# Performance work log

Measured on AMD Instinct MI355X. Metric: run time of the kernel, lower is better.

## Reference

```python
import jax, jax.numpy as jnp
import numpy as np

POOL = 7                     # cfg.POOLING_SIZE
PRE = 2 * POOL               # pre_pool_size (max_pool=True path)
LEVEL_HW = (256, 128, 64, 32)  # square H=W of P2..P5 for a 1024x1024 image


def setup_inputs() -> dict:
    key = jax.random.key(0)
    ks = jax.random.split(key, 8)
    C = 256
    feats = {f"p{i + 2}": jax.random.normal(ks[i], (1, C, s, s), dtype=jnp.float32)
             for i, s in enumerate(LEVEL_HW)}
    N = 1000
    IMG = 1024.0
    x1 = jax.random.uniform(ks[4], (N,), minval=0.0, maxval=IMG - 33.0)
    y1 = jax.random.uniform(ks[5], (N,), minval=0.0, maxval=IMG - 33.0)
    w = jax.random.uniform(ks[6], (N,), minval=32.0, maxval=512.0)
    h = jax.random.uniform(ks[7], (N,), minval=32.0, maxval=512.0)
    x2 = jnp.minimum(x1 + w, IMG - 1.0)
    y2 = jnp.minimum(y1 + h, IMG - 1.0)
    rois = jnp.stack([jnp.zeros((N,), jnp.float32), x1, y1, x2, y2], axis=1)
    inp = dict(feats)
    inp["rois"] = rois
    return inp


def _crop_pool_fpn(p2, p3, p4, p5, rois):
    """Faithful vectorized version of Network._crop_pool_layer_fpn (max_pool=True).

    Per-ROI FPN level select, affine-grid + bilinear grid_sample
    (align_corners=True semantics, zeros padding), then 2x2 max pool.
    """
    levels = (p2, p3, p4, p5)
    C = p2.shape[1]
    Hm = p2.shape[2]  # largest (P2) map; all levels padded up to this
    # Pad every level into one [L, Hm, Wm, C] array (NHWC for clean gathers).
    feats = jnp.stack([
        jnp.pad(jnp.transpose(f[0], (1, 2, 0)),
                ((0, Hm - f.shape[2]), (0, Hm - f.shape[3]), (0, 0)))
        for f in levels])

    x1, y1, x2, y2 = rois[:, 1], rois[:, 2], rois[:, 3], rois[:, 4]
    w = jnp.where(x2 - x1 <= 0, 1e-14, x2 - x1)
    h = jnp.where(y2 - y1 <= 0, 1e-14, y2 - y1)
    kf = 4.0 + jnp.log2(jnp.sqrt(w * h) / 224.0)   # k0 + log2(sqrt(wh)/224)
    kf = jnp.clip(kf, 2.0, 5.0)                     # clamp BEFORE round (as in source)
    k = jnp.round(kf)
    scale = 2.0 ** k
    lvl = k.astype(jnp.int32) - 2                   # [N] in [0,4)
    x1s, y1s, x2s, y2s = x1 / scale, y1 / scale, x2 / scale, y2 / scale

    # affine_grid(theta) + align_corners=True grid_sample collapses to direct
    # pixel coords: px = (x1+x2)/2 + t*(x2-x1)/2, t = linspace(-1, 1, PRE).
    t = jnp.linspace(-1.0, 1.0, PRE)
    px = (x1s + x2s)[:, None] * 0.5 + t[None, :] * ((x2s - x1s)[:, None] * 0.5)  # [N,PRE]
    py = (y1s + y2s)[:, None] * 0.5 + t[None, :] * ((y2s - y1s)[:, None] * 0.5)
    PX = jnp.broadcast_to(px[:, None, :], (px.shape[0], PRE, PRE))  # [N,PRE,PRE]
    PY = jnp.broadcast_to(py[:, :, None], (py.shape[0], PRE, PRE))

    HWl = jnp.asarray(LEVEL_HW, jnp.float32)[lvl][:, None, None]  # per-ROI level size (square)
    x0 = jnp.floor(PX)
    y0 = jnp.floor(PY)
    dx = PX - x0
    dy = PY - y0

    def gather(yi, xi):
        inb = ((xi >= 0) & (xi < HWl) & (yi >= 0) & (yi < HWl)).astype(feats.dtype)
        yc = jnp.clip(yi, 0, Hm - 1).astype(jnp.int32)
        xc = jnp.clip(xi, 0, Hm - 1).astype(jnp.int32)
        v = feats[lvl[:, None, None], yc, xc]      # [N,PRE,PRE,C]
        return v * inb[..., None]                   # zeros padding

    out = (gather(y0, x0) * ((1 - dy) * (1 - dx))[..., None]
           + gather(y0, x0 + 1) * ((1 - dy) * dx)[..., None]
           + gather(y0 + 1, x0) * (dy * (1 - dx))[..., None]
           + gather(y0 + 1, x0 + 1) * (dy * dx)[..., None])  # [N,PRE,PRE,C]

    crops = jnp.transpose(out, (0, 3, 1, 2))        # [N,C,PRE,PRE]
    N = crops.shape[0]
    crops = crops.reshape(N, C, POOL, 2, POOL, 2).max(axis=(3, 5))  # 2x2 max pool
    return crops                                     # [N,C,POOL,POOL]


def reference(p2, p3, p4, p5, rois):
    return _crop_pool_fpn(p2, p3, p4, p5, rois)
```

## Files before the change

### kernel.cpp

```cpp
#include <hip/hip_runtime.h>
#include <math.h>

#define C_CH 256
#define PRE 14
#define NPOOL 7
#define PIX (NPOOL * NPOOL)
#define OUT_PER_ROI (C_CH * PIX)
#define HALF_OUT (128 * PIX)
#define SROW 132

#define OFF_P2 0
#define OFF_P3 16777216u
#define OFF_P4 20971520u
#define OFF_P5 22020096u
#define WS_ELEMS 22282240u

#define RB 528

static __device__ __forceinline__ unsigned short f2bf(float f) {
    unsigned int u = __float_as_uint(f);
    unsigned int r = (u + 0x7FFFu + ((u >> 16) & 1u)) >> 16;
    return (unsigned short)r;
}
static __device__ __forceinline__ float bfLO(unsigned int u) { return __uint_as_float(u << 16); }
static __device__ __forceinline__ float bfHI(unsigned int u) { return __uint_as_float(u & 0xFFFF0000u); }

static __device__ __forceinline__ void bilerp8(uint4 a00, uint4 a01, uint4 a10, uint4 a11,
                                               float4 w, float4& lo, float4& hi) {
    lo.x = fmaf(bfLO(a00.x), w.x, fmaf(bfLO(a01.x), w.y, fmaf(bfLO(a10.x), w.z, bfLO(a11.x) * w.w)));
    lo.y = fmaf(bfHI(a00.x), w.x, fmaf(bfHI(a01.x), w.y, fmaf(bfHI(a10.x), w.z, bfHI(a11.x) * w.w)));
    lo.z = fmaf(bfLO(a00.y), w.x, fmaf(bfLO(a01.y), w.y, fmaf(bfLO(a10.y), w.z, bfLO(a11.y) * w.w)));
    lo.w = fmaf(bfHI(a00.y), w.x, fmaf(bfHI(a01.y), w.y, fmaf(bfHI(a10.y), w.z, bfHI(a11.y) * w.w)));
    hi.x = fmaf(bfLO(a00.z), w.x, fmaf(bfLO(a01.z), w.y, fmaf(bfLO(a10.z), w.z, bfLO(a11.z) * w.w)));
    hi.y = fmaf(bfHI(a00.z), w.x, fmaf(bfHI(a01.z), w.y, fmaf(bfHI(a10.z), w.z, bfHI(a11.z) * w.w)));
    hi.z = fmaf(bfLO(a00.w), w.x, fmaf(bfLO(a01.w), w.y, fmaf(bfLO(a10.w), w.z, bfLO(a11.w) * w.w)));
    hi.w = fmaf(bfHI(a00.w), w.x, fmaf(bfHI(a01.w), w.y, fmaf(bfHI(a10.w), w.z, bfHI(a11.w) * w.w)));
}

__global__ __launch_bounds__(256) void transpose_all_k(
    const float* __restrict__ p2, const float* __restrict__ p3,
    const float* __restrict__ p4, const float* __restrict__ p5,
    unsigned short* __restrict__ ws) {
    __shared__ unsigned char lds[128 * RB];

    int b = blockIdx.x;
    const float* __restrict__ src;
    int HW2; unsigned int off;
    if (b < 512)      { src = p2; HW2 = 65536; off = OFF_P2; }
    else if (b < 640) { src = p3; HW2 = 16384; off = OFF_P3; b -= 512; }
    else if (b < 672) { src = p4; HW2 = 4096;  off = OFF_P4; b -= 640; }
    else              { src = p5; HW2 = 1024;  off = OFF_P5; b -= 672; }
    const int hw0 = b << 7;

    const int t   = threadIdx.x;
    const int hwq = t & 31;
    const int cg  = t >> 5;
    const int key = (hwq & 7) << 4;

    #pragma unroll
    for (int s = 0; s < 8; ++s) {
        const int c0 = (cg << 2) + (s << 5);
        const float* g = src + (size_t)c0 * HW2 + hw0 + (hwq << 2);
        const float4 a0 = *(const float4*)(g);
        const float4 a1 = *(const float4*)(g + HW2);
        const float4 a2 = *(const float4*)(g + 2 * (size_t)HW2);
        const float4 a3 = *(const float4*)(g + 3 * (size_t)HW2);
        const int cb = (c0 << 1) ^ key;
        unsigned char* base = &lds[(hwq << 2) * RB + cb];
        ushort4 w;
        w.x = f2bf(a0.x); w.y = f2bf(a1.x); w.z = f2bf(a2.x); w.w = f2bf(a3.x);
        *(ushort4*)(base) = w;
        w.x = f2bf(a0.y); w.y = f2bf(a1.y); w.z = f2bf(a2.y); w.w = f2bf(a3.y);
        *(ushort4*)(base + RB) = w;
        w.x = f2bf(a0.z); w.y = f2bf(a1.z); w.z = f2bf(a2.z); w.w = f2bf(a3.z);
        *(ushort4*)(base + 2 * RB) = w;
        w.x = f2bf(a0.w); w.y = f2bf(a1.w); w.z = f2bf(a2.w); w.w = f2bf(a3.w);
        *(ushort4*)(base + 3 * RB) = w;
    }
    __syncthreads();

    char* __restrict__ dstb = (char*)(ws + off + ((size_t)hw0 << 8));
    const int chunk = t & 31;
    const int hwl   = t >> 5;
    #pragma unroll
    for (int p = 0; p < 16; ++p) {
        const int hw = (p << 3) + hwl;
        const int k2 = ((hw >> 2) & 7) << 4;
        const uint4 v = *(const uint4*)&lds[hw * RB + ((chunk << 4) ^ k2)];
        *(uint4*)(dstb + hw * 512 + (chunk << 4)) = v;
    }
}

template <bool HWC>
__global__ __launch_bounds__(256, 4) void roi_align_k(
    const float* __restrict__ p2, const float* __restrict__ p3,
    const float* __restrict__ p4, const float* __restrict__ p5,
    const unsigned short* __restrict__ ws, const float* __restrict__ rois,
    float* __restrict__ out) {

    __shared__ float sxw0[PRE], sxw1[PRE], syw0[PRE], syw1[PRE];
    __shared__ int   sxc0[PRE], sxc1[PRE], syc0[PRE], syc1[PRE];
    __shared__ float4 wtab[PRE * PRE];
    __shared__ int4   otab[PRE * PRE];
    __shared__ float  sout[PIX * SROW];

    const int n   = blockIdx.x;
    const int ch0 = blockIdx.y << 7;
    const float x1 = rois[n * 5 + 1];
    const float y1 = rois[n * 5 + 2];
    const float x2 = rois[n * 5 + 3];
    const float y2 = rois[n * 5 + 4];

    float w = x2 - x1; w = (w <= 0.f) ? 1e-14f : w;
    float h = y2 - y1; h = (h <= 0.f) ? 1e-14f : h;
    float kf = 4.f + log2f(sqrtf(w * h) * (1.f / 224.f));
    kf = fminf(fmaxf(kf, 2.f), 5.f);
    const float kr = rintf(kf);
    const int   lvl = (int)kr - 2;
    const float scale = exp2f(kr);
    const int   HW = 256 >> lvl;

    const int t = threadIdx.x;

    if (t < 2 * PRE) {
        const bool isx = t < PRE;
        const int  j = isx ? t : t - PRE;
        const float a1 = isx ? x1 : y1;
        const float a2 = isx ? x2 : y2;
        const float a1s = a1 / scale, a2s = a2 / scale;
        const float cen  = (a1s + a2s) * 0.5f;
        const float half = (a2s - a1s) * 0.5f;
        const float tt = -1.f + (2.f / 13.f) * (float)j;
        const float p  = cen + tt * half;
        const float p0 = floorf(p);
        const float d  = p - p0;
        const float HWf = (float)HW;
        const float m0 = (p0 >= 0.f && p0 < HWf) ? 1.f : 0.f;
        const float m1 = (p0 + 1.f >= 0.f && p0 + 1.f < HWf) ? 1.f : 0.f;
        const int c0i = min(max((int)p0, 0), HW - 1);
        const int c1i = min(max((int)p0 + 1, 0), HW - 1);
        if (isx) { sxw0[j] = (1.f - d) * m0; sxw1[j] = d * m1; sxc0[j] = c0i; sxc1[j] = c1i; }
        else     { syw0[j] = (1.f - d) * m0; syw1[j] = d * m1; syc0[j] = c0i; syc1[j] = c1i; }
    }
    __syncthreads();

    if (HWC) {
        for (int s = t; s < PRE * PRE; s += 256) {
            const int i = s / PRE;
            const int j = s - i * PRE;
            wtab[s] = make_float4(syw0[i] * sxw0[j], syw0[i] * sxw1[j],
                                  syw1[i] * sxw0[j], syw1[i] * sxw1[j]);
            otab[s] = make_int4((syc0[i] * HW + sxc0[j]) << 9, (syc0[i] * HW + sxc1[j]) << 9,
                                (syc1[i] * HW + sxc0[j]) << 9, (syc1[i] * HW + sxc1[j]) << 9);
        }
        __syncthreads();
    }

    if (HWC) {
        const int g   = t & 15;
        const int ph  = t >> 4;
        const unsigned int off = (lvl == 0) ? OFF_P2 : (lvl == 1) ? OFF_P3 : (lvl == 2) ? OFF_P4 : OFF_P5;
        const char* __restrict__ base = (const char*)(ws + off);
        const int cb2 = (ch0 + (g << 3)) << 1;

        #define DO_PIXEL(P)                                                           \
        {                                                                             \
            const int p_ = (P);                                                       \
            const int oy_ = p_ / 7;                                                   \
            const int ox_ = p_ - oy_ * 7;                                             \
            const int s00 = oy_ * 28 + (ox_ << 1);                                    \
            const int4  oA = otab[s00];      const float4 wA = wtab[s00];             \
            const int4  oB = otab[s00 + 1];  const float4 wB = wtab[s00 + 1];         \
            const int4  oC = otab[s00 + 14]; const float4 wC = wtab[s00 + 14];        \
            const int4  oD = otab[s00 + 15]; const float4 wD = wtab[s00 + 15];        \
            const uint4 A00 = *(const uint4*)(base + (oA.x + cb2));                   \
            const uint4 A01 = *(const uint4*)(base + (oA.y + cb2));                   \
            const uint4 A10 = *(const uint4*)(base + (oA.z + cb2));                   \
            const uint4 A11 = *(const uint4*)(base + (oA.w + cb2));                   \
            const uint4 B00 = *(const uint4*)(base + (oB.x + cb2));                   \
            const uint4 B01 = *(const uint4*)(base + (oB.y + cb2));                   \
            const uint4 B10 = *(const uint4*)(base + (oB.z + cb2));                   \
            const uint4 B11 = *(const uint4*)(base + (oB.w + cb2));                   \
            const uint4 C00 = *(const uint4*)(base + (oC.x + cb2));                   \
            const uint4 C01 = *(const uint4*)(base + (oC.y + cb2));                   \
            const uint4 C10 = *(const uint4*)(base + (oC.z + cb2));                   \
            const uint4 C11 = *(const uint4*)(base + (oC.w + cb2));                   \
            const uint4 D00 = *(const uint4*)(base + (oD.x + cb2));                   \
            const uint4 D01 = *(const uint4*)(base + (oD.y + cb2));                   \
            const uint4 D10 = *(const uint4*)(base + (oD.z + cb2));                   \
            const uint4 D11 = *(const uint4*)(base + (oD.w + cb2));                   \
            float4 aLo, aHi, bLo, bHi, cLo, cHi, dLo, dHi;                            \
            bilerp8(A00, A01, A10, A11, wA, aLo, aHi);                                \
            bilerp8(B00, B01, B10, B11, wB, bLo, bHi);                                \
            bilerp8(C00, C01, C10, C11, wC, cLo, cHi);                                \
            bilerp8(D00, D01, D10, D11, wD, dLo, dHi);                                \
            float4 mLo, mHi;                                                          \
            mLo.x = fmaxf(fmaxf(aLo.x, bLo.x), fmaxf(cLo.x, dLo.x));                  \
            mLo.y = fmaxf(fmaxf(aLo.y, bLo.y), fmaxf(cLo.y, dLo.y));                  \
            mLo.z = fmaxf(fmaxf(aLo.z, bLo.z), fmaxf(cLo.z, dLo.z));                  \
            mLo.w = fmaxf(fmaxf(aLo.w, bLo.w), fmaxf(cLo.w, dLo.w));                  \
            mHi.x = fmaxf(fmaxf(aHi.x, bHi.x), fmaxf(cHi.x, dHi.x));                  \
            mHi.y = fmaxf(fmaxf(aHi.y, bHi.y), fmaxf(cHi.y, dHi.y));                  \
            mHi.z = fmaxf(fmaxf(aHi.z, bHi.z), fmaxf(cHi.z, dHi.z));                  \
            mHi.w = fmaxf(fmaxf(aHi.w, bHi.w), fmaxf(cHi.w, dHi.w));                  \
            *(float4*)&sout[p_ * SROW + (g << 3)] = mLo;                              \
            *(float4*)&sout[p_ * SROW + (g << 3) + 4] = mHi;                          \
        }

        DO_PIXEL(ph)
        DO_PIXEL(ph + 16)
        DO_PIXEL(ph + 32)
        if (ph == 0) DO_PIXEL(48)
        #undef DO_PIXEL
    } else {
        const int g     = t & 31;
        const int s     = t >> 5;
        const int cbase = ch0 + (g << 2);
        const float* __restrict__ fbF = (lvl == 0) ? p2 : (lvl == 1) ? p3 : (lvl == 2) ? p4 : p5;
        const int HW2 = HW * HW;
        for (int p = s; p < PIX; p += 8) {
            const int oy = p / 7;
            const int ox = p - oy * 7;
            float4 m = make_float4(-3.4e38f, -3.4e38f, -3.4e38f, -3.4e38f);
            #pragma unroll
            for (int sy = 0; sy < 2; ++sy) {
                const int i = oy * 2 + sy;
                const float wy0 = syw0[i], wy1 = syw1[i];
                const int   yc0 = syc0[i], yc1 = syc1[i];
                #pragma unroll
                for (int sx = 0; sx < 2; ++sx) {
                    const int j = ox * 2 + sx;
                    const float w00 = wy0 * sxw0[j], w01 = wy0 * sxw1[j];
                    const float w10 = wy1 * sxw0[j], w11 = wy1 * sxw1[j];
                    const int   xc0 = sxc0[j], xc1 = sxc1[j];
                    float vv[4];
                    #pragma unroll
                    for (int k = 0; k < 4; ++k) {
                        const size_t cb = (size_t)(cbase + k) * HW2;
                        const float a00 = fbF[cb + yc0 * HW + xc0];
                        const float a01 = fbF[cb + yc0 * HW + xc1];
                        const float a10 = fbF[cb + yc1 * HW + xc0];
                        const float a11 = fbF[cb + yc1 * HW + xc1];
                        vv[k] = fmaf(a00, w00, fmaf(a01, w01, fmaf(a10, w10, a11 * w11)));
                    }
                    m.x = fmaxf(m.x, vv[0]);
                    m.y = fmaxf(m.y, vv[1]);
                    m.z = fmaxf(m.z, vv[2]);
                    m.w = fmaxf(m.w, vv[3]);
                }
            }
            *(float4*)&sout[p * SROW + (g << 2)] = m;
        }
    }
    __syncthreads();

    const size_t ob = (size_t)n * OUT_PER_ROI + (size_t)ch0 * PIX;
    for (int o = t; o < HALF_OUT; o += 256) {
        const int c  = o / PIX;
        const int pp = o - c * PIX;
        out[ob + o] = sout[pp * SROW + c];
    }
}

extern "C" void kernel_launch(void* const* d_in, const int* in_sizes, int n_in,
                              void* d_out, int out_size, void* d_ws, size_t ws_size,
                              hipStream_t stream) {
    const float* p2   = (const float*)d_in[0];
    const float* p3   = (const float*)d_in[1];
    const float* p4   = (const float*)d_in[2];
    const float* p5   = (const float*)d_in[3];
    const float* rois = (const float*)d_in[4];
    float* out = (float*)d_out;
    const int N = in_sizes[4] / 5;

    const size_t need = (size_t)WS_ELEMS * sizeof(unsigned short);
    if (ws_size >= need) {
        unsigned short* ws = (unsigned short*)d_ws;
        transpose_all_k<<<680, 256, 0, stream>>>(p2, p3, p4, p5, ws);
        roi_align_k<true><<<dim3(N, 2), 256, 0, stream>>>(p2, p3, p4, p5, ws, rois, out);
    } else {
        roi_align_k<false><<<dim3(N, 2), 256, 0, stream>>>(p2, p3, p4, p5, nullptr, rois, out);
    }
}
```

Measured before the change: 49.74 us.

## Sort ROIs by level and position for cache-local gathers

An extra block in the transpose kernel computes each ROI's pyramid level and top-left cell, then bitonic-sorts ROIs by (level, y, x) in shared memory and writes a permutation. The ROI-align kernel reads that permutation and interleaves sorted positions across 8 groups (matching XCD round-robin dispatch), so spatially nearby ROIs run on the same XCD and share L2. The aim is better L2 reuse of the bf16 feature gathers. The cost is a serial sort block that can extend the transpose kernel's tail, plus one extra indirection per block.

```diff
diff --git a/kernel.cpp b/kernel.cpp
--- a/kernel.cpp
+++ b/kernel.cpp
@@ -16,6 +16,7 @@
 #define WS_ELEMS 22282240u
 
 #define RB 528
+#define NTRANS 680
 
 static __device__ __forceinline__ unsigned short f2bf(float f) {
     unsigned int u = __float_as_uint(f);
@@ -40,8 +41,49 @@
 __global__ __launch_bounds__(256) void transpose_all_k(
     const float* __restrict__ p2, const float* __restrict__ p3,
     const float* __restrict__ p4, const float* __restrict__ p5,
-    unsigned short* __restrict__ ws) {
+    unsigned short* __restrict__ ws, const float* __restrict__ rois,
+    unsigned* __restrict__ perm, int N) {
     __shared__ unsigned char lds[128 * RB];
+
+    if (blockIdx.x == NTRANS) {
+        unsigned long long* kv = (unsigned long long*)lds;
+        const int t = threadIdx.x;
+        for (int i = t; i < 1024; i += 256) {
+            unsigned key = 0xFFFFFFFFu;
+            if (i < N) {
+                const float x1 = rois[i * 5 + 1];
+                const float y1 = rois[i * 5 + 2];
+                const float x2 = rois[i * 5 + 3];
+                const float y2 = rois[i * 5 + 4];
+                float w = x2 - x1; w = (w <= 0.f) ? 1e-14f : w;
+                float h = y2 - y1; h = (h <= 0.f) ? 1e-14f : h;
+                float kf = 4.f + log2f(sqrtf(w * h) * (1.f / 224.f));
+                kf = fminf(fmaxf(kf, 2.f), 5.f);
+                const float kr = rintf(kf);
+                const int lvl = (int)kr - 2;
+                const float inv = exp2f(-kr);
+                const int yi = (int)(y1 * inv);
+                const int xi = (int)(x1 * inv);
+                key = ((unsigned)lvl << 26) | ((unsigned)yi << 13) | (unsigned)xi;
+            }
+            kv[i] = ((unsigned long long)key << 32) | (unsigned)i;
+        }
+        __syncthreads();
+        for (int k = 2; k <= 1024; k <<= 1) {
+            for (int j = k >> 1; j > 0; j >>= 1) {
+                for (int i = t; i < 512; i += 256) {
+                    const int e = (i << 1) - (i & (j - 1));
+                    const int f = e | j;
+                    const bool up = ((e & k) == 0);
+                    const unsigned long long A = kv[e], B = kv[f];
+                    if ((A > B) == up) { kv[e] = B; kv[f] = A; }
+                }
+                __syncthreads();
+            }
+        }
+        for (int i = t; i < N; i += 256) perm[i] = (unsigned)kv[i];
+        return;
+    }
 
     int b = blockIdx.x;
     const float* __restrict__ src;
@@ -96,7 +138,7 @@
     const float* __restrict__ p2, const float* __restrict__ p3,
     const float* __restrict__ p4, const float* __restrict__ p5,
     const unsigned short* __restrict__ ws, const float* __restrict__ rois,
-    float* __restrict__ out) {
+    const unsigned* __restrict__ perm, int N, float* __restrict__ out) {
 
     __shared__ float sxw0[PRE], sxw1[PRE], syw0[PRE], syw1[PRE];
     __shared__ int   sxc0[PRE], sxc1[PRE], syc0[PRE], syc1[PRE];
@@ -104,7 +146,16 @@
     __shared__ int4   otab[PRE * PRE];
     __shared__ float  sout[PIX * SROW];
 
-    const int n   = blockIdx.x;
+    int n;
+    if (HWC) {
+        const int bid = blockIdx.x;
+        int spos;
+        if ((N & 7) == 0) spos = (bid & 7) * (N >> 3) + (bid >> 3);
+        else              spos = bid;
+        n = (int)perm[spos];
+    } else {
+        n = blockIdx.x;
+    }
     const int ch0 = blockIdx.y << 7;
     const float x1 = rois[n * 5 + 1];
     const float y1 = rois[n * 5 + 2];
@@ -273,12 +324,13 @@
     float* out = (float*)d_out;
     const int N = in_sizes[4] / 5;
 
-    const size_t need = (size_t)WS_ELEMS * sizeof(unsigned short);
-    if (ws_size >= need) {
+    const size_t need = (size_t)WS_ELEMS * sizeof(unsigned short) + 4096;
+    if (ws_size >= need && N <= 1024) {
         unsigned short* ws = (unsigned short*)d_ws;
-        transpose_all_k<<<680, 256, 0, stream>>>(p2, p3, p4, p5, ws);
-        roi_align_k<true><<<dim3(N, 2), 256, 0, stream>>>(p2, p3, p4, p5, ws, rois, out);
+        unsigned* perm = (unsigned*)((char*)d_ws + (size_t)WS_ELEMS * sizeof(unsigned short));
+        transpose_all_k<<<NTRANS + 1, 256, 0, stream>>>(p2, p3, p4, p5, ws, rois, perm, N);
+        roi_align_k<true><<<dim3(N, 2), 256, 0, stream>>>(p2, p3, p4, p5, ws, rois, perm, N, out);
     } else {
-        roi_align_k<false><<<dim3(N, 2), 256, 0, stream>>>(p2, p3, p4, p5, nullptr, rois, out);
-    }
-}
+        roi_align_k<false><<<dim3(N, 2), 256, 0, stream>>>(p2, p3, p4, p5, nullptr, rois, nullptr, N, out);
+    }
+}
```

Result: slower. 60.64 us (+21.9%).
